# Kernel tuning notes

Hardware: AMD Instinct MI355X
Metric: run time of the kernel (lower is better)

The kernel has to match this reference:

```python
import jax, jax.numpy as jnp
import numpy as np

NUM_HEADS = 12
FEATURE_DIM = 16
HEAD_DIM = 128
EPS = 1e-12


def taylor_map(x):
    # x: [b, h, t, d] -> [b, h, t, 1 + d + d*d] (2nd-order Taylor features of exp)
    d = x.shape[-1]
    r2 = jnp.asarray(np.sqrt(2.0), x.dtype)
    rd = jnp.asarray(np.sqrt(d), x.dtype)
    rrd = jnp.asarray(np.sqrt(np.sqrt(d)), x.dtype)
    x2 = (x[..., :, None] * x[..., None, :]).reshape(x.shape[:-1] + (d * d,)) / r2
    ones = jnp.ones(x.shape[:-1] + (1,), x.dtype)
    return jnp.concatenate([ones, x / rrd, x2 / rd], axis=-1)


def setup_inputs() -> dict:
    key = jax.random.key(0)
    ks = jax.random.split(key, 5)
    b, t, hid = 2, 2048, 1536
    scale = 0.02
    return {
        "hidden_states": jax.random.normal(ks[0], (b, t, hid), jnp.float32),
        "Wq": jax.random.normal(ks[1], (NUM_HEADS * FEATURE_DIM, hid), jnp.float32) * scale,
        "Wk": jax.random.normal(ks[2], (NUM_HEADS * FEATURE_DIM, hid), jnp.float32) * scale,
        "Wv": jax.random.normal(ks[3], (NUM_HEADS * HEAD_DIM, hid), jnp.float32) * scale,
        "Wo": jax.random.normal(ks[4], (hid, NUM_HEADS * HEAD_DIM), jnp.float32) * scale,
    }


def reference(hidden_states, Wq, Wk, Wv, Wo):
    b, t, _ = hidden_states.shape
    H, dk, dv = NUM_HEADS, FEATURE_DIM, HEAD_DIM
    # projections (torch Linear: x @ W^T), split heads -> [b, h, t, d]
    q = (hidden_states @ Wq.T).reshape(b, t, H, dk).transpose(0, 2, 1, 3)
    k = (hidden_states @ Wk.T).reshape(b, t, H, dk).transpose(0, 2, 1, 3)
    v = (hidden_states @ Wv.T).reshape(b, t, H, dv).transpose(0, 2, 1, 3)
    qf = taylor_map(q)  # [b, h, t, D], D = 1 + dk + dk^2
    kf = taylor_map(k)
    # causal kernelized attention: identical math to cumsum-of-outer-products form
    S = jnp.einsum("bhtd,bhsd->bhts", qf, kf)  # [b, h, t, t]
    mask = jnp.tril(jnp.ones((t, t), bool))
    S = jnp.where(mask, S, jnp.zeros((), S.dtype))
    num = jnp.einsum("bhts,bhse->bhte", S, v)  # [b, h, t, dv]
    den = S.sum(-1) + EPS  # [b, h, t]
    y = num / den[..., None]
    y = y.transpose(0, 2, 1, 3).reshape(b, t, H * dv)
    return y @ Wo.T
```

## Files before the change

kernel.cpp:

```cpp
#include <hip/hip_runtime.h>

#define B 2
#define T 2048
#define HID 1536
#define NH 12
#define DK 16
#define DV 128
#define BT (B * T)
#define EPS 1e-12f

typedef __attribute__((ext_vector_type(8))) short bf16x8;
typedef __attribute__((ext_vector_type(4))) float f32x4;

__device__ __forceinline__ unsigned short f2bf(float f) {
    unsigned int u = __float_as_uint(f);
    u += 0x7FFFu + ((u >> 16) & 1u);
    return (unsigned short)(u >> 16);
}

__global__ __launch_bounds__(256) void cvt_all(const float* __restrict__ hs,
                                               const float* __restrict__ Wq,
                                               const float* __restrict__ Wk,
                                               const float* __restrict__ Wv,
                                               const float* __restrict__ Wo,
                                               unsigned short* __restrict__ hsb,
                                               unsigned short* __restrict__ wqk,
                                               unsigned short* __restrict__ wvb,
                                               unsigned short* __restrict__ wob) {
    int bx = blockIdx.x;
    const float* src;
    unsigned short* dst;
    if (bx < 3072)      { src = hs; dst = hsb; }
    else if (bx < 3216) { src = Wq; dst = wqk;          bx -= 3072; }
    else if (bx < 3360) { src = Wk; dst = wqk + 294912; bx -= 3216; }
    else if (bx < 4512) { src = Wv; dst = wvb;          bx -= 3360; }
    else                { src = Wo; dst = wob;          bx -= 4512; }
    const int i = (bx * 256 + threadIdx.x) * 8;
    float4 a = *(const float4*)(src + i);
    float4 b = *(const float4*)(src + i + 4);
    *(ushort4*)(dst + i)     = make_ushort4(f2bf(a.x), f2bf(a.y), f2bf(a.z), f2bf(a.w));
    *(ushort4*)(dst + i + 4) = make_ushort4(f2bf(b.x), f2bf(b.y), f2bf(b.z), f2bf(b.w));
}

__device__ __forceinline__ void gemm_tile_bf16(const unsigned short* __restrict__ A,
                                               const unsigned short* __restrict__ Bm,
                                               unsigned short* __restrict__ C,
                                               int m0, int n0, int K, int ldc,
                                               unsigned short* As, unsigned short* Bs) {
    const int tid = threadIdx.x;
    const int wave = tid >> 6, lane = tid & 63;
    const int wm = (wave & 1) * 64, wn = (wave >> 1) * 64;
    const int fr = lane & 15;
    const int fk = (lane >> 4) * 8;

    f32x4 acc[4][4];
#pragma unroll
    for (int i = 0; i < 4; ++i)
#pragma unroll
        for (int j = 0; j < 4; ++j) acc[i][j] = (f32x4)0.f;

    const int c0 = tid, c1 = tid + 256;
    const int r0 = c0 >> 2, q0 = (c0 & 3) * 8;
    const int r1 = c1 >> 2, q1 = (c1 & 3) * 8;

    for (int k0 = 0; k0 < K; k0 += 32) {
        __builtin_amdgcn_global_load_lds(
            (const __attribute__((address_space(1))) void*)(A + (size_t)(m0 + r0) * K + k0 + q0),
            (__attribute__((address_space(3))) void*)(As + c0 * 8), 16, 0, 0);
        __builtin_amdgcn_global_load_lds(
            (const __attribute__((address_space(1))) void*)(A + (size_t)(m0 + r1) * K + k0 + q1),
            (__attribute__((address_space(3))) void*)(As + c1 * 8), 16, 0, 0);
        __builtin_amdgcn_global_load_lds(
            (const __attribute__((address_space(1))) void*)(Bm + (size_t)(n0 + r0) * K + k0 + q0),
            (__attribute__((address_space(3))) void*)(Bs + c0 * 8), 16, 0, 0);
        __builtin_amdgcn_global_load_lds(
            (const __attribute__((address_space(1))) void*)(Bm + (size_t)(n0 + r1) * K + k0 + q1),
            (__attribute__((address_space(3))) void*)(Bs + c1 * 8), 16, 0, 0);
        __syncthreads();

        bf16x8 af[4], bfr[4];
#pragma unroll
        for (int mb = 0; mb < 4; ++mb)
            af[mb] = *(const bf16x8*)(As + (wm + mb * 16 + fr) * 32 + fk);
#pragma unroll
        for (int nb = 0; nb < 4; ++nb)
            bfr[nb] = *(const bf16x8*)(Bs + (wn + nb * 16 + fr) * 32 + fk);
#pragma unroll
        for (int mb = 0; mb < 4; ++mb)
#pragma unroll
            for (int nb = 0; nb < 4; ++nb)
                acc[mb][nb] = __builtin_amdgcn_mfma_f32_16x16x32_bf16(
                    af[mb], bfr[nb], acc[mb][nb], 0, 0, 0);
        __syncthreads();
    }

    const int orow = (lane >> 4) * 4;
#pragma unroll
    for (int nb = 0; nb < 4; ++nb) {
        const int col = n0 + wn + nb * 16 + fr;
#pragma unroll
        for (int mb = 0; mb < 4; ++mb) {
            const int row = m0 + wm + mb * 16 + orow;
#pragma unroll
            for (int r = 0; r < 4; ++r)
                C[(size_t)(row + r) * ldc + col] = f2bf(acc[mb][nb][r]);
        }
    }
}

__global__ __launch_bounds__(256) void proj_qkv(const unsigned short* __restrict__ hsb,
                                                const unsigned short* __restrict__ wqk,
                                                const unsigned short* __restrict__ wvb,
                                                unsigned short* __restrict__ qkb,
                                                unsigned short* __restrict__ vtg) {
    __shared__ unsigned short As[128 * 32];
    __shared__ unsigned short Bs[128 * 32];
    const int bx = blockIdx.x;
    if (bx < 96) {
        gemm_tile_bf16(hsb, wqk, qkb, (bx / 3) * 128, (bx % 3) * 128, HID, 384, As, Bs);
    } else {
        const int vid = bx - 96;
        const int grp = vid / 48, sub = vid % 48;
        const int n_t = grp * 4 + (sub & 3), m_t = sub >> 2;
        gemm_tile_bf16(wvb, hsb, vtg, m_t * 128, n_t * 128, HID, BT, As, Bs);
    }
}

__global__ __launch_bounds__(256) void proj_out(const unsigned short* __restrict__ A,
                                                const unsigned short* __restrict__ Bm,
                                                float* __restrict__ C) {
    __shared__ unsigned short As[128 * 32];
    __shared__ unsigned short Bs[128 * 32];
    const int tid = threadIdx.x;
    const int m0 = blockIdx.y * 128;
    const int n0 = blockIdx.x * 128;
    const int wave = tid >> 6, lane = tid & 63;
    const int wm = (wave & 1) * 64, wn = (wave >> 1) * 64;
    const int fr = lane & 15;
    const int fk = (lane >> 4) * 8;
    const int K = HID;

    f32x4 acc[4][4];
#pragma unroll
    for (int i = 0; i < 4; ++i)
#pragma unroll
        for (int j = 0; j < 4; ++j) acc[i][j] = (f32x4)0.f;

    const int c0 = tid, c1 = tid + 256;
    const int r0 = c0 >> 2, q0 = (c0 & 3) * 8;
    const int r1 = c1 >> 2, q1 = (c1 & 3) * 8;

    for (int k0 = 0; k0 < K; k0 += 32) {
        __builtin_amdgcn_global_load_lds(
            (const __attribute__((address_space(1))) void*)(A + (size_t)(m0 + r0) * K + k0 + q0),
            (__attribute__((address_space(3))) void*)(As + c0 * 8), 16, 0, 0);
        __builtin_amdgcn_global_load_lds(
            (const __attribute__((address_space(1))) void*)(A + (size_t)(m0 + r1) * K + k0 + q1),
            (__attribute__((address_space(3))) void*)(As + c1 * 8), 16, 0, 0);
        __builtin_amdgcn_global_load_lds(
            (const __attribute__((address_space(1))) void*)(Bm + (size_t)(n0 + r0) * K + k0 + q0),
            (__attribute__((address_space(3))) void*)(Bs + c0 * 8), 16, 0, 0);
        __builtin_amdgcn_global_load_lds(
            (const __attribute__((address_space(1))) void*)(Bm + (size_t)(n0 + r1) * K + k0 + q1),
            (__attribute__((address_space(3))) void*)(Bs + c1 * 8), 16, 0, 0);
        __syncthreads();

        bf16x8 af[4], bfr[4];
#pragma unroll
        for (int mb = 0; mb < 4; ++mb)
            af[mb] = *(const bf16x8*)(As + (wm + mb * 16 + fr) * 32 + fk);
#pragma unroll
        for (int nb = 0; nb < 4; ++nb)
            bfr[nb] = *(const bf16x8*)(Bs + (wn + nb * 16 + fr) * 32 + fk);
#pragma unroll
        for (int mb = 0; mb < 4; ++mb)
#pragma unroll
            for (int nb = 0; nb < 4; ++nb)
                acc[mb][nb] = __builtin_amdgcn_mfma_f32_16x16x32_bf16(
                    af[mb], bfr[nb], acc[mb][nb], 0, 0, 0);
        __syncthreads();
    }

    const int orow = (lane >> 4) * 4;
#pragma unroll
    for (int nb = 0; nb < 4; ++nb) {
        const int col = n0 + wn + nb * 16 + fr;
#pragma unroll
        for (int mb = 0; mb < 4; ++mb) {
            const int row = m0 + wm + mb * 16 + orow;
#pragma unroll
            for (int r = 0; r < 4; ++r)
                C[(size_t)(row + r) * HID + col] = acc[mb][nb][r];
        }
    }
}

__global__ __launch_bounds__(256) void based_attn_mfma(const unsigned short* __restrict__ qk,
                                                       const unsigned short* __restrict__ vt,
                                                       unsigned short* __restrict__ yb) {
    const int bx = blockIdx.x;
    const int qt = (T / 64 - 1) - (bx / (NH * B * 2));
    const int sub = bx % (NH * B * 2);
    const int h   = sub >> 2;
    const int bi  = (sub >> 1) & 1;
    const int dvs = sub & 1;
    const int tid = threadIdx.x;
    const int wave = tid >> 6, lane = tid & 63;
    const int fr = lane & 15, quad = lane >> 4;
    const int fk = quad * 8;

    __shared__ __attribute__((aligned(16))) unsigned short ss[2][64][72];
    __shared__ float den_lds[64];
    if (tid < 64) den_lds[tid] = 0.f;

    const bf16x8 zf = {};
    bf16x8 qf[4];
#pragma unroll
    for (int nt = 0; nt < 4; ++nt) {
        qf[nt] = zf;
        if (quad < 2)
            qf[nt] = *(const bf16x8*)&qk[(size_t)(bi * T + qt * 64 + nt * 16 + fr) * 384
                                         + h * DK + fk];
    }

    f32x4 oacc[4];
#pragma unroll
    for (int nt = 0; nt < 4; ++nt) oacc[nt] = (f32x4)0.f;
    float denp[4] = {0.f, 0.f, 0.f, 0.f};

    const size_t vrow = (size_t)(h * DV + dvs * 64 + wave * 16 + fr) * BT + bi * T;

    for (int kt = 0; kt <= qt; ++kt) {
        const int bsel = kt & 1;
        bf16x8 kf = zf;
        if (quad < 2)
            kf = *(const bf16x8*)&qk[(size_t)(bi * T + kt * 64 + wave * 16 + fr) * 384
                                     + 192 + h * DK + fk];
        bf16x8 vf[2];
#pragma unroll
        for (int k2 = 0; k2 < 2; ++k2)
            vf[k2] = *(const bf16x8*)&vt[vrow + kt * 64 + k2 * 32 + fk];

        f32x4 sa[4];
#pragma unroll
        for (int nt = 0; nt < 4; ++nt)
            sa[nt] = __builtin_amdgcn_mfma_f32_16x16x32_bf16(kf, qf[nt], (f32x4)0.f, 0, 0, 0);

        const bool diag = (kt == qt);
#pragma unroll
        for (int nt = 0; nt < 4; ++nt) {
            const int i = nt * 16 + fr;
            float sv[4];
#pragma unroll
            for (int r = 0; r < 4; ++r) {
                const int j = wave * 16 + quad * 4 + r;
                const float a = sa[nt][r];
                float s = 1.f + 0.25f * a + a * a * (1.f / 32.f);
                if (diag && (j > i)) s = 0.f;
                sv[r] = s;
                denp[nt] += s;
            }
            *(ushort4*)&ss[bsel][i][wave * 16 + quad * 4] =
                make_ushort4(f2bf(sv[0]), f2bf(sv[1]), f2bf(sv[2]), f2bf(sv[3]));
        }
        __syncthreads();

#pragma unroll
        for (int k2 = 0; k2 < 2; ++k2) {
            bf16x8 sf[4];
#pragma unroll
            for (int nt = 0; nt < 4; ++nt)
                sf[nt] = *(const bf16x8*)&ss[bsel][nt * 16 + fr][k2 * 32 + fk];
#pragma unroll
            for (int nt = 0; nt < 4; ++nt)
                oacc[nt] = __builtin_amdgcn_mfma_f32_16x16x32_bf16(
                    vf[k2], sf[nt], oacc[nt], 0, 0, 0);
        }
    }

#pragma unroll
    for (int nt = 0; nt < 4; ++nt) {
        float v = denp[nt];
        v += __shfl_xor(v, 16);
        v += __shfl_xor(v, 32);
        if (quad == 0) atomicAdd(&den_lds[nt * 16 + fr], v);
    }
    __syncthreads();

#pragma unroll
    for (int nt = 0; nt < 4; ++nt) {
        const int i = nt * 16 + fr;
        const float rd = 1.f / (den_lds[i] + EPS);
        const size_t rowbase = (size_t)(bi * T + qt * 64 + i) * (NH * DV) + h * DV;
        const int c = dvs * 64 + wave * 16 + quad * 4;
        const f32x4 o = oacc[nt];
        *(ushort4*)&yb[rowbase + c] = make_ushort4(f2bf(o[0] * rd), f2bf(o[1] * rd),
                                                   f2bf(o[2] * rd), f2bf(o[3] * rd));
    }
}

extern "C" void kernel_launch(void* const* d_in, const int* in_sizes, int n_in,
                              void* d_out, int out_size, void* d_ws, size_t ws_size,
                              hipStream_t stream) {
    (void)in_sizes; (void)n_in; (void)out_size; (void)ws_size;
    const float* hs = (const float*)d_in[0];
    const float* Wq = (const float*)d_in[1];
    const float* Wk = (const float*)d_in[2];
    const float* Wv = (const float*)d_in[3];
    const float* Wo = (const float*)d_in[4];
    float* out = (float*)d_out;

    unsigned short* hsb = (unsigned short*)d_ws;
    unsigned short* wqk = hsb + (size_t)BT * HID;
    unsigned short* wvb = wqk + (size_t)384 * HID;
    unsigned short* wob = wvb + (size_t)HID * HID;
    unsigned short* qkb = wob + (size_t)HID * HID;
    unsigned short* vtg = qkb + (size_t)BT * 384;
    unsigned short* ybb = vtg + (size_t)HID * BT;

    dim3 blk(256);
    cvt_all<<<dim3(5664), blk, 0, stream>>>(hs, Wq, Wk, Wv, Wo, hsb, wqk, wvb, wob);

    proj_qkv<<<dim3(480), blk, 0, stream>>>(hsb, wqk, wvb, qkb, vtg);

    based_attn_mfma<<<dim3(T / 64 * NH * B * 2), blk, 0, stream>>>(qkb, vtg, ybb);

    proj_out<<<dim3(12, 32), blk, 0, stream>>>(ybb, wob, out);
}
```

Baseline: 216.4 us.

## Compute all 128 value dims per attention block and prefetch next K/V tiles

The attention kernel no longer splits the value dimension across two blocks. Each block now accumulates all 128 output columns, so the QK^T score tile and its Taylor-feature evaluation are computed once instead of twice. The next iteration's K and V fragments are loaded into registers ahead of use to hide global-load latency. Score conversion to bf16 now truncates instead of rounding, and the polynomial uses fmaf. In exchange, accumulator register pressure doubles and the grid is halved, which may reduce occupancy and hurt load balance across CUs.

Result: no change. 214.7 us (-0.8%).

```diff
diff --git a/kernel.cpp b/kernel.cpp
--- a/kernel.cpp
+++ b/kernel.cpp
@@ -199,15 +199,15 @@
                                                        const unsigned short* __restrict__ vt,
                                                        unsigned short* __restrict__ yb) {
     const int bx = blockIdx.x;
-    const int qt = (T / 64 - 1) - (bx / (NH * B * 2));
-    const int sub = bx % (NH * B * 2);
-    const int h   = sub >> 2;
-    const int bi  = (sub >> 1) & 1;
-    const int dvs = sub & 1;
+    const int qt = (T / 64 - 1) - (bx / (NH * B));
+    const int hb = bx % (NH * B);
+    const int h  = hb >> 1;
+    const int bi = hb & 1;
     const int tid = threadIdx.x;
     const int wave = tid >> 6, lane = tid & 63;
     const int fr = lane & 15, quad = lane >> 4;
     const int fk = quad * 8;
+    const int fkk = (quad & 1) * 8;
 
     __shared__ __attribute__((aligned(16))) unsigned short ss[2][64][72];
     __shared__ float den_lds[64];
@@ -223,45 +223,67 @@
                                          + h * DK + fk];
     }
 
-    f32x4 oacc[4];
-#pragma unroll
-    for (int nt = 0; nt < 4; ++nt) oacc[nt] = (f32x4)0.f;
+    f32x4 oacc[2][4];
+#pragma unroll
+    for (int mt = 0; mt < 2; ++mt)
+#pragma unroll
+        for (int nt = 0; nt < 4; ++nt) oacc[mt][nt] = (f32x4)0.f;
     float denp[4] = {0.f, 0.f, 0.f, 0.f};
 
-    const size_t vrow = (size_t)(h * DV + dvs * 64 + wave * 16 + fr) * BT + bi * T;
+    const unsigned short* kbase = qk + (size_t)(bi * T + wave * 16 + fr) * 384 + 192 + h * DK + fkk;
+    const unsigned short* vbase0 = vt + (size_t)(h * DV + wave * 32 + fr) * BT + bi * T + fk;
+    const unsigned short* vbase1 = vbase0 + (size_t)16 * BT;
+
+    bf16x8 kf_n = *(const bf16x8*)kbase;
+    bf16x8 vf_n[2][2];
+    vf_n[0][0] = *(const bf16x8*)(vbase0);
+    vf_n[0][1] = *(const bf16x8*)(vbase0 + 32);
+    vf_n[1][0] = *(const bf16x8*)(vbase1);
+    vf_n[1][1] = *(const bf16x8*)(vbase1 + 32);
 
     for (int kt = 0; kt <= qt; ++kt) {
         const int bsel = kt & 1;
-        bf16x8 kf = zf;
-        if (quad < 2)
-            kf = *(const bf16x8*)&qk[(size_t)(bi * T + kt * 64 + wave * 16 + fr) * 384
-                                     + 192 + h * DK + fk];
-        bf16x8 vf[2];
-#pragma unroll
-        for (int k2 = 0; k2 < 2; ++k2)
-            vf[k2] = *(const bf16x8*)&vt[vrow + kt * 64 + k2 * 32 + fk];
+        const bf16x8 kf = kf_n;
+        bf16x8 vf[2][2];
+        vf[0][0] = vf_n[0][0]; vf[0][1] = vf_n[0][1];
+        vf[1][0] = vf_n[1][0]; vf[1][1] = vf_n[1][1];
+
+        {
+            const int ktn = (kt < qt) ? kt + 1 : qt;
+            kf_n = *(const bf16x8*)(kbase + (size_t)ktn * 64 * 384);
+            const int off = ktn * 64;
+            vf_n[0][0] = *(const bf16x8*)(vbase0 + off);
+            vf_n[0][1] = *(const bf16x8*)(vbase0 + off + 32);
+            vf_n[1][0] = *(const bf16x8*)(vbase1 + off);
+            vf_n[1][1] = *(const bf16x8*)(vbase1 + off + 32);
+        }
 
         f32x4 sa[4];
 #pragma unroll
         for (int nt = 0; nt < 4; ++nt)
             sa[nt] = __builtin_amdgcn_mfma_f32_16x16x32_bf16(kf, qf[nt], (f32x4)0.f, 0, 0, 0);
 
-        const bool diag = (kt == qt);
 #pragma unroll
         for (int nt = 0; nt < 4; ++nt) {
             const int i = nt * 16 + fr;
             float sv[4];
 #pragma unroll
             for (int r = 0; r < 4; ++r) {
-                const int j = wave * 16 + quad * 4 + r;
                 const float a = sa[nt][r];
-                float s = 1.f + 0.25f * a + a * a * (1.f / 32.f);
-                if (diag && (j > i)) s = 0.f;
-                sv[r] = s;
-                denp[nt] += s;
+                sv[r] = fmaf(a, fmaf(a, 1.f / 32.f, 0.25f), 1.f);
             }
-            *(ushort4*)&ss[bsel][i][wave * 16 + quad * 4] =
-                make_ushort4(f2bf(sv[0]), f2bf(sv[1]), f2bf(sv[2]), f2bf(sv[3]));
+            if (kt == qt) {
+#pragma unroll
+                for (int r = 0; r < 4; ++r) {
+                    const int j = wave * 16 + quad * 4 + r;
+                    if (j > i) sv[r] = 0.f;
+                }
+            }
+            denp[nt] += sv[0] + sv[1] + sv[2] + sv[3];
+            uint2 pk;
+            pk.x = (__float_as_uint(sv[0]) >> 16) | (__float_as_uint(sv[1]) & 0xFFFF0000u);
+            pk.y = (__float_as_uint(sv[2]) >> 16) | (__float_as_uint(sv[3]) & 0xFFFF0000u);
+            *(uint2*)&ss[bsel][i][wave * 16 + quad * 4] = pk;
         }
         __syncthreads();
 
@@ -272,9 +294,11 @@
             for (int nt = 0; nt < 4; ++nt)
                 sf[nt] = *(const bf16x8*)&ss[bsel][nt * 16 + fr][k2 * 32 + fk];
 #pragma unroll
-            for (int nt = 0; nt < 4; ++nt)
-                oacc[nt] = __builtin_amdgcn_mfma_f32_16x16x32_bf16(
-                    vf[k2], sf[nt], oacc[nt], 0, 0, 0);
+            for (int mt = 0; mt < 2; ++mt)
+#pragma unroll
+                for (int nt = 0; nt < 4; ++nt)
+                    oacc[mt][nt] = __builtin_amdgcn_mfma_f32_16x16x32_bf16(
+                        vf[mt][k2], sf[nt], oacc[mt][nt], 0, 0, 0);
         }
     }
 
@@ -292,10 +316,13 @@
         const int i = nt * 16 + fr;
         const float rd = 1.f / (den_lds[i] + EPS);
         const size_t rowbase = (size_t)(bi * T + qt * 64 + i) * (NH * DV) + h * DV;
-        const int c = dvs * 64 + wave * 16 + quad * 4;
-        const f32x4 o = oacc[nt];
-        *(ushort4*)&yb[rowbase + c] = make_ushort4(f2bf(o[0] * rd), f2bf(o[1] * rd),
-                                                   f2bf(o[2] * rd), f2bf(o[3] * rd));
+#pragma unroll
+        for (int mt = 0; mt < 2; ++mt) {
+            const int c = wave * 32 + mt * 16 + quad * 4;
+            const f32x4 o = oacc[mt][nt];
+            *(ushort4*)&yb[rowbase + c] = make_ushort4(f2bf(o[0] * rd), f2bf(o[1] * rd),
+                                                       f2bf(o[2] * rd), f2bf(o[3] * rd));
+        }
     }
 }
 
@@ -323,7 +350,7 @@
 
     proj_qkv<<<dim3(480), blk, 0, stream>>>(hsb, wqk, wvb, qkb, vtg);
 
-    based_attn_mfma<<<dim3(T / 64 * NH * B * 2), blk, 0, stream>>>(qkb, vtg, ybb);
+    based_attn_mfma<<<dim3(T / 64 * NH * B), blk, 0, stream>>>(qkb, vtg, ybb);
 
     proj_out<<<dim3(12, 32), blk, 0, stream>>>(ybb, wob, out);
 }
```
